# Kernel tuning notes

Hardware: AMD Instinct MI355X
Metric: run time of the kernel (lower is better)

## Reference

```python
import jax, jax.numpy as jnp
import numpy as np
import math

VOCAB = 128
READ_DIM = 128
LOGIT_SCALE = 1.0 / 16.0
NUM_FF = 6
CARRY_DIM = 896
D_MODEL = CARRY_DIM + READ_DIM


def ste_sign(x):
    # forward of the STE sign: +-1, zero -> +1
    return jnp.where(x >= 0, 1.0, -1.0).astype(x.dtype)


def ste_round(x):
    return jnp.round(x)


def setup_inputs() -> dict:
    key = jax.random.key(0)
    k_tok, k_init, k_emb, k_ff, k_head, k_thr = jax.random.split(key, 6)
    tokens = jax.random.randint(k_tok, (64, 512), 0, VOCAB, dtype=jnp.int64) if jax.config.read('jax_enable_x64') else jax.random.randint(k_tok, (64, 512), 0, VOCAB, dtype=jnp.int32)
    initial_lat = jax.random.uniform(k_init, (D_MODEL,), minval=-1.0, maxval=1.0)
    embed_lat = jax.random.uniform(k_emb, (VOCAB, READ_DIM), minval=-1.0, maxval=1.0)
    ff_lat = jax.random.uniform(k_ff, (NUM_FF, D_MODEL, D_MODEL), minval=-1.0, maxval=1.0)
    head_lat = jax.random.uniform(k_head, (READ_DIM, VOCAB), minval=-1.0, maxval=1.0)
    ff_thresh_lat = jax.random.uniform(k_thr, (NUM_FF, D_MODEL), minval=-2.0, maxval=2.0)
    return {
        'tokens': tokens,
        'initial_lat': initial_lat,
        'embed_lat': embed_lat,
        'ff_lat': ff_lat,
        'head_lat': head_lat,
        'ff_thresh_lat': ff_thresh_lat,
    }


def reference(tokens, initial_lat, embed_lat, ff_lat, head_lat, ff_thresh_lat):
    B, T = tokens.shape
    num_ff = ff_lat.shape[0]
    d_model = initial_lat.shape[0]
    carry_dim = d_model - READ_DIM
    act_scale = math.sqrt(d_model)

    initial = ste_sign(initial_lat)          # [d_model]
    embed = ste_sign(embed_lat)              # [VOCAB, read_dim]
    ff = ste_sign(ff_lat)                    # [num_ff, d_model, d_model]
    head = ste_sign(head_lat)                # [read_dim, VOCAB]
    thr = ste_round(ff_thresh_lat)           # [num_ff, d_model]

    x0 = jnp.broadcast_to(initial[None, :], (B, d_model))

    def step(x, tok_t):
        # tok_t: [B]
        h = x
        for i in range(num_ff):
            pre = h @ ff[i]                  # [B, d_model]
            h = ste_sign((pre - thr[i]) / act_scale)
        carry = h[:, :carry_dim]
        read = h[:, carry_dim:]
        logits = read @ head * LOGIT_SCALE   # [B, VOCAB]
        logp = jax.nn.log_softmax(logits, axis=-1)
        loss_t = -jnp.mean(jnp.take_along_axis(logp, tok_t[:, None], axis=1))
        x_new = jnp.concatenate([carry, embed[tok_t]], axis=1)
        return x_new, loss_t

    _, losses = jax.lax.scan(step, x0, tokens.T)  # scan over T
    return jnp.mean(losses)
```

## Files before the change

### kernel.cpp

```cpp
#include <hip/hip_runtime.h>
#include <stdint.h>

typedef unsigned long long u64;

#define VOCAB 128
#define RD 128
#define DM 1024
#define NFF 6
#define BATCH 64
#define TSTEPS 512
#define THR 512

#define OFF_EB    786432
#define OFF_HB    788480
#define OFF_LOSS  790528

typedef const __attribute__((address_space(1))) void* gas1_t;
typedef __attribute__((address_space(3))) void*       las3_t;

__global__ void pack_ff(const float* __restrict__ ff, u64* __restrict__ ffs) {
    int wid  = blockIdx.x * (blockDim.x >> 6) + (threadIdx.x >> 6);
    int lane = threadIdx.x & 63;
    int jt = wid & 15;
    int w  = (wid >> 4) & 15;
    int L  = wid >> 8;
    int j  = jt * 64 + lane;
    const float* src = ff + ((size_t)(L * DM) + w * 64) * DM + j;
    u64 word = 0;
#pragma unroll
    for (int b = 0; b < 64; ++b) {
        float v = src[(size_t)b * DM];
        word |= (u64)(v < 0.0f) << b;
    }
    int half = j >> 9, c = j & 511, q = w >> 1, s = w & 1;
    ffs[((((L * 2 + half) * 8 + q) * 512 + c) << 1) + s] = word;
}

__global__ void pack_small(const float* __restrict__ emb, const float* __restrict__ head,
                           u64* __restrict__ eb, u64* __restrict__ hb) {
    int tid = threadIdx.x;
    if (tid < 128) {
        int v = tid;
        for (int wd = 0; wd < 2; ++wd) {
            u64 word = 0;
            for (int l = 0; l < 64; ++l)
                word |= (u64)(emb[v * RD + wd * 64 + l] < 0.0f) << l;
            eb[v * 2 + wd] = word;
        }
    } else {
        int v = tid - 128;
        for (int wd = 0; wd < 2; ++wd) {
            u64 word = 0;
            for (int l = 0; l < 64; ++l)
                word |= (u64)(head[(wd * 64 + l) * VOCAB + v] < 0.0f) << l;
            hb[v * 2 + wd] = word;
        }
    }
}

#define ISSUE(L, H, NB)                                                        \
    do {                                                                       \
        const u64* gp_ = ffs + (((L) * 2 + (H)) * 8192) + (wv << 10) + (lane << 1); \
        u64* lp_ = sbuf + ((NB) * 8192 + (wv << 10));                          \
        _Pragma("unroll")                                                      \
        for (int k_ = 0; k_ < 8; ++k_) {                                       \
            __builtin_amdgcn_global_load_lds((gas1_t)(gp_ + (k_ << 7)),        \
                                             (las3_t)(lp_ + (k_ << 7)), 16, 0, 0); \
        }                                                                      \
    } while (0)

#define CSTAGE(L, H, NB)                                                       \
    do {                                                                       \
        const ulonglong2* hp_ = (const ulonglong2*)hx[(L) & 1];                \
        const u64* wb_ = sbuf + ((NB) * 8192 + (tid << 1));                    \
        int acc_ = 0;                                                          \
        _Pragma("unroll")                                                      \
        for (int q_ = 0; q_ < 8; ++q_) {                                       \
            ulonglong2 hv_ = hp_[q_];              \
            ulonglong2 wq_ = *(const ulonglong2*)(wb_ + (q_ << 10));           \
            acc_ += __popcll(hv_.x ^ wq_.x) + __popcll(hv_.y ^ wq_.y);         \
        }                                                                      \
        u64 m_ = __ballot(acc_ >= cthr[L][H]);                                 \
        if (lane == 0) hx[((L) + 1) & 1][(H) * 8 + wv] = m_;                   \
    } while (0)

#define SBAR()                                                                  \
    do {                                                                        \
        asm volatile("s_waitcnt vmcnt(0) lgkmcnt(0)" ::: "memory");             \
        __builtin_amdgcn_s_barrier();                                           \
    } while (0)

#define BARRIER()                                                               \
    do {                                                                        \
        asm volatile("s_waitcnt lgkmcnt(0)" ::: "memory");                      \
        __builtin_amdgcn_s_barrier();                                           \
    } while (0)

__global__ void __launch_bounds__(THR)
brnn_main(const int* __restrict__ tokens,
          const float* __restrict__ initial_lat,
          const float* __restrict__ thr_lat,
          const u64* __restrict__ ffs,
          const u64* __restrict__ eb,
          const u64* __restrict__ hb,
          double* __restrict__ losses)
{
    const int b    = blockIdx.x;
    const int tid  = threadIdx.x;
    const int lane = tid & 63;
    const int wv   = tid >> 6;

    __shared__ __align__(16) u64 sbuf[2 * 8192];
    __shared__ __align__(16) u64 hx[2][16];
    __shared__ u64 hbL[2 * VOCAB];

    if (tid < 2 * VOCAB) hbL[tid] = hb[tid];

    int cthr[NFF][2];
#pragma unroll
    for (int L = 0; L < NFF; ++L)
#pragma unroll
        for (int h2 = 0; h2 < 2; ++h2) {
            int th = (int)rintf(thr_lat[L * DM + h2 * 512 + tid]);
            cthr[L][h2] = ((DM - th) >> 1) + 1;
        }

    {
        u64 m0 = __ballot(initial_lat[tid] < 0.0f);
        u64 m1 = __ballot(initial_lat[512 + tid] < 0.0f);
        if (lane == 0) { hx[0][wv] = m0; hx[0][8 + wv] = m1; }
    }

    ISSUE(0, 0, 0);
    asm volatile("s_waitcnt vmcnt(0)" ::: "memory");
    __syncthreads();

    const int* toks = tokens + b * TSTEPS;
    double lacc = 0.0;

    for (int t = 0; t < TSTEPS; ++t) {
        const int tok = toks[t];
        u64 enew = 0;
        if (wv == 0 && lane < 2) enew = eb[tok * 2 + lane];

        ISSUE(0, 1, 1); CSTAGE(0, 0, 0); SBAR();
        ISSUE(1, 0, 0); CSTAGE(0, 1, 1); SBAR();
        ISSUE(1, 1, 1); CSTAGE(1, 0, 0); SBAR();
        ISSUE(2, 0, 0); CSTAGE(1, 1, 1); SBAR();
        ISSUE(2, 1, 1); CSTAGE(2, 0, 0); SBAR();
        ISSUE(3, 0, 0); CSTAGE(2, 1, 1); SBAR();
        ISSUE(3, 1, 1); CSTAGE(3, 0, 0); SBAR();
        ISSUE(4, 0, 0); CSTAGE(3, 1, 1); SBAR();
        ISSUE(4, 1, 1); CSTAGE(4, 0, 0); SBAR();
        ISSUE(5, 0, 0); CSTAGE(4, 1, 1); SBAR();
        ISSUE(5, 1, 1); CSTAGE(5, 0, 0); SBAR();
        ISSUE(0, 0, 0); CSTAGE(5, 1, 1); SBAR();

        if (wv == 0) {
            u64 ra = hx[0][14], rb = hx[0][15];
            u64 h0a = hbL[lane * 2 + 0],        h0b = hbL[lane * 2 + 1];
            u64 h1a = hbL[(lane + 64) * 2 + 0], h1b = hbL[(lane + 64) * 2 + 1];
            int d0 = 128 - 2 * (__popcll(ra ^ h0a) + __popcll(rb ^ h0b));
            int d1 = 128 - 2 * (__popcll(ra ^ h1a) + __popcll(rb ^ h1b));
            float l0 = (float)d0 * (1.0f / 16.0f);
            float l1 = (float)d1 * (1.0f / 16.0f);
            float mx = fmaxf(l0, l1);
#pragma unroll
            for (int sh = 32; sh >= 1; sh >>= 1) mx = fmaxf(mx, __shfl_xor(mx, sh));
            float se = __expf(l0 - mx) + __expf(l1 - mx);
#pragma unroll
            for (int sh = 32; sh >= 1; sh >>= 1) se += __shfl_xor(se, sh);
            int   tl   = tok & 63;
            float la   = __shfl(l0, tl);
            float lb   = __shfl(l1, tl);
            float ltok = (tok >> 6) ? lb : la;
            lacc += (double)(mx + __logf(se) - ltok);
            if (lane < 2) hx[0][14 + lane] = enew;
        }
        BARRIER();
    }

    if (tid == 0) losses[b] = lacc;
}

__global__ void reduce_loss(const double* __restrict__ losses, float* __restrict__ out) {
    int lane = threadIdx.x;
    double v = losses[lane];
#pragma unroll
    for (int sh = 32; sh >= 1; sh >>= 1) v += __shfl_down(v, sh);
    if (lane == 0) out[0] = (float)(v * (1.0 / ((double)BATCH * (double)TSTEPS)));
}

extern "C" void kernel_launch(void* const* d_in, const int* in_sizes, int n_in,
                              void* d_out, int out_size, void* d_ws, size_t ws_size,
                              hipStream_t stream) {
    const int*   tokens  = (const int*)d_in[0];
    const float* initial = (const float*)d_in[1];
    const float* embed   = (const float*)d_in[2];
    const float* ff      = (const float*)d_in[3];
    const float* head    = (const float*)d_in[4];
    const float* thrl    = (const float*)d_in[5];

    char* ws = (char*)d_ws;
    u64*    ffs    = (u64*)ws;
    u64*    eb     = (u64*)(ws + OFF_EB);
    u64*    hb     = (u64*)(ws + OFF_HB);
    double* losses = (double*)(ws + OFF_LOSS);

    pack_ff<<<384, 256, 0, stream>>>(ff, ffs);
    pack_small<<<1, 256, 0, stream>>>(embed, head, eb, hb);
    brnn_main<<<BATCH, THR, 0, stream>>>(tokens, initial, thrl, ffs, eb, hb, losses);
    reduce_loss<<<1, 64, 0, stream>>>(losses, (float*)d_out);
}
```

Baseline: 6.050 ms.

## Split binary FF stages into half-K chunks with triple-buffered two-ahead prefetch

Each layer-half matmul stage is split into two K-halves of 32 KB. The weight stream to LDS becomes a three-buffer ring that prefetches two chunks ahead, and the repack kernel reorders the packed weights to match. The barrier now waits only for the oldest outstanding load group (vmcnt(4)) instead of draining all loads, so more global-to-LDS traffic overlaps the popcount compute. The cost is twice as many workgroup barriers per timestep and a popcount accumulator carried across stages.

```diff
diff --git a/kernel.cpp b/kernel.cpp
--- a/kernel.cpp
+++ b/kernel.cpp
@@ -32,8 +32,11 @@
         float v = src[(size_t)b * DM];
         word |= (u64)(v < 0.0f) << b;
     }
-    int half = j >> 9, c = j & 511, q = w >> 1, s = w & 1;
-    ffs[((((L * 2 + half) * 8 + q) * 512 + c) << 1) + s] = word;
+    int q = w >> 1, s = w & 1;
+    int half = j >> 9, c = j & 511;
+    int kh = q >> 2, qq = q & 3;
+    int stage = L * 4 + half * 2 + kh;
+    ffs[(size_t)stage * 4096 + qq * 1024 + c * 2 + s] = word;
 }
 
 __global__ void pack_small(const float* __restrict__ emb, const float* __restrict__ head,
@@ -58,42 +61,44 @@
     }
 }
 
-#define ISSUE(L, H, NB)                                                        \
+#define ISSUE(S, B)                                                            \
     do {                                                                       \
-        const u64* gp_ = ffs + (((L) * 2 + (H)) * 8192) + (wv << 10) + (lane << 1); \
-        u64* lp_ = sbuf + ((NB) * 8192 + (wv << 10));                          \
+        const u64* gp_ = ffs + ((S) * 4096) + (wv << 9) + (lane << 1);         \
+        u64* lp_ = sbuf + ((B) * 4096) + (wv << 9);                            \
         _Pragma("unroll")                                                      \
-        for (int k_ = 0; k_ < 8; ++k_) {                                       \
+        for (int k_ = 0; k_ < 4; ++k_) {                                       \
             __builtin_amdgcn_global_load_lds((gas1_t)(gp_ + (k_ << 7)),        \
                                              (las3_t)(lp_ + (k_ << 7)), 16, 0, 0); \
         }                                                                      \
     } while (0)
 
-#define CSTAGE(L, H, NB)                                                       \
+#define STG(S)                                                                 \
     do {                                                                       \
-        const ulonglong2* hp_ = (const ulonglong2*)hx[(L) & 1];                \
-        const u64* wb_ = sbuf + ((NB) * 8192 + (tid << 1));                    \
-        int acc_ = 0;                                                          \
-        _Pragma("unroll")                                                      \
-        for (int q_ = 0; q_ < 8; ++q_) {                                       \
-            ulonglong2 hv_ = hp_[q_];              \
-            ulonglong2 wq_ = *(const ulonglong2*)(wb_ + (q_ << 10));           \
-            acc_ += __popcll(hv_.x ^ wq_.x) + __popcll(hv_.y ^ wq_.y);         \
+        ISSUE((((S) + 2) % 24), (((S) + 2) % 3));                              \
+        {                                                                      \
+            const int L_ = (S) >> 2, HALF_ = ((S) >> 1) & 1, KH_ = (S) & 1;    \
+            const ulonglong2* hp_ = (const ulonglong2*)hx[L_ & 1];             \
+            const u64* wb_ = sbuf + (((S) % 3) * 4096) + (tid << 1);           \
+            _Pragma("unroll")                                                  \
+            for (int qq_ = 0; qq_ < 4; ++qq_) {                                \
+                ulonglong2 hv_ = hp_[KH_ * 4 + qq_];       \
+                ulonglong2 wq_ = *(const ulonglong2*)(wb_ + (qq_ << 10));      \
+                acc += __popcll(hv_.x ^ wq_.x) + __popcll(hv_.y ^ wq_.y);      \
+            }                                                                  \
+            if (KH_) {                                                         \
+                u64 m_ = __ballot(acc >= cthr[L_][HALF_]);                     \
+                if (lane == 0) hx[(L_ + 1) & 1][HALF_ * 8 + wv] = m_;          \
+                acc = 0;                                                       \
+            }                                                                  \
         }                                                                      \
-        u64 m_ = __ballot(acc_ >= cthr[L][H]);                                 \
-        if (lane == 0) hx[((L) + 1) & 1][(H) * 8 + wv] = m_;                   \
+        asm volatile("s_waitcnt vmcnt(4) lgkmcnt(0)" ::: "memory");            \
+        __builtin_amdgcn_s_barrier();                                          \
     } while (0)
 
-#define SBAR()                                                                  \
-    do {                                                                        \
-        asm volatile("s_waitcnt vmcnt(0) lgkmcnt(0)" ::: "memory");             \
-        __builtin_amdgcn_s_barrier();                                           \
-    } while (0)
-
-#define BARRIER()                                                               \
-    do {                                                                        \
-        asm volatile("s_waitcnt lgkmcnt(0)" ::: "memory");                      \
-        __builtin_amdgcn_s_barrier();                                           \
+#define BARRIER()                                                              \
+    do {                                                                       \
+        asm volatile("s_waitcnt lgkmcnt(0)" ::: "memory");                     \
+        __builtin_amdgcn_s_barrier();                                          \
     } while (0)
 
 __global__ void __launch_bounds__(THR)
@@ -110,7 +115,7 @@
     const int lane = tid & 63;
     const int wv   = tid >> 6;
 
-    __shared__ __align__(16) u64 sbuf[2 * 8192];
+    __shared__ __align__(16) u64 sbuf[3 * 4096];
     __shared__ __align__(16) u64 hx[2][16];
     __shared__ u64 hbL[2 * VOCAB];
 
@@ -131,30 +136,26 @@
         if (lane == 0) { hx[0][wv] = m0; hx[0][8 + wv] = m1; }
     }
 
-    ISSUE(0, 0, 0);
-    asm volatile("s_waitcnt vmcnt(0)" ::: "memory");
-    __syncthreads();
+    ISSUE(0, 0);
+    ISSUE(1, 1);
+    asm volatile("s_waitcnt vmcnt(4) lgkmcnt(0)" ::: "memory");
+    __builtin_amdgcn_s_barrier();
 
     const int* toks = tokens + b * TSTEPS;
     double lacc = 0.0;
+    int acc = 0;
 
     for (int t = 0; t < TSTEPS; ++t) {
         const int tok = toks[t];
         u64 enew = 0;
         if (wv == 0 && lane < 2) enew = eb[tok * 2 + lane];
 
-        ISSUE(0, 1, 1); CSTAGE(0, 0, 0); SBAR();
-        ISSUE(1, 0, 0); CSTAGE(0, 1, 1); SBAR();
-        ISSUE(1, 1, 1); CSTAGE(1, 0, 0); SBAR();
-        ISSUE(2, 0, 0); CSTAGE(1, 1, 1); SBAR();
-        ISSUE(2, 1, 1); CSTAGE(2, 0, 0); SBAR();
-        ISSUE(3, 0, 0); CSTAGE(2, 1, 1); SBAR();
-        ISSUE(3, 1, 1); CSTAGE(3, 0, 0); SBAR();
-        ISSUE(4, 0, 0); CSTAGE(3, 1, 1); SBAR();
-        ISSUE(4, 1, 1); CSTAGE(4, 0, 0); SBAR();
-        ISSUE(5, 0, 0); CSTAGE(4, 1, 1); SBAR();
-        ISSUE(5, 1, 1); CSTAGE(5, 0, 0); SBAR();
-        ISSUE(0, 0, 0); CSTAGE(5, 1, 1); SBAR();
+        STG(0);  STG(1);  STG(2);  STG(3);
+        STG(4);  STG(5);  STG(6);  STG(7);
+        STG(8);  STG(9);  STG(10); STG(11);
+        STG(12); STG(13); STG(14); STG(15);
+        STG(16); STG(17); STG(18); STG(19);
+        STG(20); STG(21); STG(22); STG(23);
 
         if (wv == 0) {
             u64 ra = hx[0][14], rb = hx[0][15];
@@ -180,6 +181,7 @@
         BARRIER();
     }
 
+    asm volatile("s_waitcnt vmcnt(0)" ::: "memory");
     if (tid == 0) losses[b] = lacc;
 }
 
```

New measurement: 6.306 ms. 4.2% more time.

## Keep layer-4 packed weights resident in registers instead of streaming through LDS

Applied to the files above, without the earlier changes.

Layer 4's packed binary weights are stored in a per-thread layout and loaded once into 32 u64 registers per thread. Layer 4 is then computed straight from those registers, which removes its two global-to-LDS staging loads and merges its two half-stages into one barrier interval. The packed-weight indexing and the prefetch schedule are rewritten so that layer 5 is loaded during the register-based layer. In exchange, each thread holds 64 extra VGPRs, which adds register pressure at 512 threads per block.

```diff
diff --git a/kernel.cpp b/kernel.cpp
--- a/kernel.cpp
+++ b/kernel.cpp
@@ -32,8 +32,13 @@
         float v = src[(size_t)b * DM];
         word |= (u64)(v < 0.0f) << b;
     }
-    int half = j >> 9, c = j & 511, q = w >> 1, s = w & 1;
-    ffs[((((L * 2 + half) * 8 + q) * 512 + c) << 1) + s] = word;
+    if (L == 4) {
+        ffs[81920 + (size_t)j * 16 + w] = word;
+    } else {
+        int S = (L < 4 ? L * 2 : 8) + (j >> 9);
+        int q = w >> 1, s = w & 1, c = j & 511;
+        ffs[(size_t)S * 8192 + q * 1024 + c * 2 + s] = word;
+    }
 }
 
 __global__ void pack_small(const float* __restrict__ emb, const float* __restrict__ head,
@@ -58,10 +63,10 @@
     }
 }
 
-#define ISSUE(L, H, NB)                                                        \
+#define ISSUE(S, B)                                                            \
     do {                                                                       \
-        const u64* gp_ = ffs + (((L) * 2 + (H)) * 8192) + (wv << 10) + (lane << 1); \
-        u64* lp_ = sbuf + ((NB) * 8192 + (wv << 10));                          \
+        const u64* gp_ = ffs + ((S) * 8192) + (wv << 10) + (lane << 1);        \
+        u64* lp_ = sbuf + ((B) * 8192 + (wv << 10));                           \
         _Pragma("unroll")                                                      \
         for (int k_ = 0; k_ < 8; ++k_) {                                       \
             __builtin_amdgcn_global_load_lds((gas1_t)(gp_ + (k_ << 7)),        \
@@ -69,10 +74,10 @@
         }                                                                      \
     } while (0)
 
-#define CSTAGE(L, H, NB)                                                       \
+#define CSTAGE(L, H, B)                                                        \
     do {                                                                       \
         const ulonglong2* hp_ = (const ulonglong2*)hx[(L) & 1];                \
-        const u64* wb_ = sbuf + ((NB) * 8192 + (tid << 1));                    \
+        const u64* wb_ = sbuf + ((B) * 8192 + (tid << 1));                     \
         int acc_ = 0;                                                          \
         _Pragma("unroll")                                                      \
         for (int q_ = 0; q_ < 8; ++q_) {                                       \
@@ -116,6 +121,15 @@
 
     if (tid < 2 * VOCAB) hbL[tid] = hb[tid];
 
+    u64 fr0[16], fr1[16];
+#pragma unroll
+    for (int w = 0; w < 16; ++w) {
+        u64 v0 = ffs[81920 + (size_t)tid * 16 + w];
+        u64 v1 = ffs[81920 + (size_t)(tid + 512) * 16 + w];
+        asm volatile("" : "+v"(v0), "+v"(v1));
+        fr0[w] = v0; fr1[w] = v1;
+    }
+
     int cthr[NFF][2];
 #pragma unroll
     for (int L = 0; L < NFF; ++L)
@@ -131,7 +145,7 @@
         if (lane == 0) { hx[0][wv] = m0; hx[0][8 + wv] = m1; }
     }
 
-    ISSUE(0, 0, 0);
+    ISSUE(0, 0);
     asm volatile("s_waitcnt vmcnt(0)" ::: "memory");
     __syncthreads();
 
@@ -143,18 +157,34 @@
         u64 enew = 0;
         if (wv == 0 && lane < 2) enew = eb[tok * 2 + lane];
 
-        ISSUE(0, 1, 1); CSTAGE(0, 0, 0); SBAR();
-        ISSUE(1, 0, 0); CSTAGE(0, 1, 1); SBAR();
-        ISSUE(1, 1, 1); CSTAGE(1, 0, 0); SBAR();
-        ISSUE(2, 0, 0); CSTAGE(1, 1, 1); SBAR();
-        ISSUE(2, 1, 1); CSTAGE(2, 0, 0); SBAR();
-        ISSUE(3, 0, 0); CSTAGE(2, 1, 1); SBAR();
-        ISSUE(3, 1, 1); CSTAGE(3, 0, 0); SBAR();
-        ISSUE(4, 0, 0); CSTAGE(3, 1, 1); SBAR();
-        ISSUE(4, 1, 1); CSTAGE(4, 0, 0); SBAR();
-        ISSUE(5, 0, 0); CSTAGE(4, 1, 1); SBAR();
-        ISSUE(5, 1, 1); CSTAGE(5, 0, 0); SBAR();
-        ISSUE(0, 0, 0); CSTAGE(5, 1, 1); SBAR();
+        ISSUE(1, 1); CSTAGE(0, 0, 0); SBAR();
+        ISSUE(2, 0); CSTAGE(0, 1, 1); SBAR();
+        ISSUE(3, 1); CSTAGE(1, 0, 0); SBAR();
+        ISSUE(4, 0); CSTAGE(1, 1, 1); SBAR();
+        ISSUE(5, 1); CSTAGE(2, 0, 0); SBAR();
+        ISSUE(6, 0); CSTAGE(2, 1, 1); SBAR();
+        ISSUE(7, 1); CSTAGE(3, 0, 0); SBAR();
+        ISSUE(8, 0); CSTAGE(3, 1, 1); SBAR();
+
+        ISSUE(9, 1);
+        {
+            const ulonglong2* hp = (const ulonglong2*)hx[0];
+            int a0 = 0, a1 = 0;
+#pragma unroll
+            for (int q = 0; q < 8; ++q) {
+                ulonglong2 hv = hp[q];
+                a0 += __popcll(hv.x ^ fr0[2 * q]) + __popcll(hv.y ^ fr0[2 * q + 1]);
+                a1 += __popcll(hv.x ^ fr1[2 * q]) + __popcll(hv.y ^ fr1[2 * q + 1]);
+            }
+            u64 m0 = __ballot(a0 >= cthr[4][0]);
+            u64 m1 = __ballot(a1 >= cthr[4][1]);
+            if (lane == 0) { hx[1][wv] = m0; hx[1][8 + wv] = m1; }
+        }
+        BARRIER();
+
+        CSTAGE(5, 0, 0); SBAR();
+        ISSUE(0, 0);
+        CSTAGE(5, 1, 1); SBAR();
 
         if (wv == 0) {
             u64 ra = hx[0][14], rb = hx[0][15];
@@ -180,6 +210,7 @@
         BARRIER();
     }
 
+    asm volatile("s_waitcnt vmcnt(0)" ::: "memory");
     if (tid == 0) losses[b] = lacc;
 }
 
```

Result: slower. 6.345 ms (+4.9%).
